# Optimization experiments

Hardware: AMD Instinct MI355X
Metric: run time of the kernel (lower is better)

## Reference

```python
import jax, jax.numpy as jnp
import numpy as np

N_NODES = 100000


def gcn_conv(x, src, dst, W, b, num_nodes):
    # PyG GCNConv: add self-loops, symmetric normalization D^-1/2 (A+I) D^-1/2, then linear.
    loop = jnp.arange(num_nodes, dtype=src.dtype)
    s = jnp.concatenate([src, loop])
    d = jnp.concatenate([dst, loop])
    deg = jax.ops.segment_sum(jnp.ones_like(d, dtype=x.dtype), d, num_segments=num_nodes)
    dinv = jnp.where(deg > 0, jax.lax.rsqrt(deg), 0.0)
    norm = dinv[s] * dinv[d]                       # [E+N]
    h = x @ W                                      # [N, out]
    msg = h[s] * norm[:, None]                     # gather + scale
    out = jax.ops.segment_sum(msg, d, num_segments=num_nodes)  # scatter-add
    return out + b


def setup_inputs() -> dict:
    key = jax.random.key(0)
    k1, k2, k3, k4 = jax.random.split(key, 4)
    F_IN, HID, C = 165, 128, 2
    E = 3200000
    x = jax.random.normal(k1, (N_NODES, F_IN), dtype=jnp.float32)
    edge_index = jax.random.randint(k2, (2, E), 0, N_NODES, dtype=jnp.int64)
    W1 = jax.random.normal(k3, (F_IN, HID), dtype=jnp.float32) * (1.0 / np.sqrt(F_IN))
    b1 = jnp.zeros((HID,), dtype=jnp.float32)
    W2 = jax.random.normal(k4, (HID, C), dtype=jnp.float32) * (1.0 / np.sqrt(HID))
    b2 = jnp.zeros((C,), dtype=jnp.float32)
    return {"x": x, "edge_index": edge_index, "W1": W1, "b1": b1, "W2": W2, "b2": b2}


def reference(x, edge_index, W1, b1, W2, b2):
    src, dst = edge_index[0], edge_index[1]
    h = jax.nn.relu(gcn_conv(x, src, dst, W1, b1, N_NODES))
    # dropout is identity in eval mode (self.training=False)
    out = gcn_conv(h, src, dst, W2, b2, N_NODES)
    return out
```

## Files before the change

kernel.cpp:

```cpp
#include <hip/hip_runtime.h>

#define NN  100000
#define FIN 165
#define HID 128
#define NBUCK 391
#define CHUNK 8192
#define CAP   9216
#define KPAD 192
#define WS   196

typedef __attribute__((ext_vector_type(4))) float f32x4;
typedef __attribute__((ext_vector_type(8))) short short8;

#define OFF_DINV   0
#define OFF_H1     100352
#define OFF_Z      (OFF_H1 + NN * 64)
#define OFF_ROWPTR (OFF_Z + 2 * NN)
#define OFF_GBASE  (OFF_ROWPTR + 100352)
#define OFF_GCUR   (OFF_GBASE + 512)
#define OFF_BUCK   (OFF_GCUR + 512)
#define OFF_EDATA  (OFF_BUCK + NBUCK * CAP)
#define OFF_WTHI   (OFF_EDATA + 3200000)

__device__ __forceinline__ unsigned bf16rne(float f) {
    unsigned u = __float_as_uint(f);
    return (u + 0x7FFFu + ((u >> 16) & 1u)) >> 16;
}

__device__ __forceinline__ float2 bf2_to_f2(unsigned int u) {
    float2 r;
    r.x = __uint_as_float(u << 16);
    r.y = __uint_as_float(u & 0xffff0000u);
    return r;
}

__device__ __forceinline__ short8 ldfrag(const ushort* p) {
    union { uint2 u[2]; short8 s; } f;
    f.u[0] = *(const uint2*)p;
    f.u[1] = *(const uint2*)(p + 16);
    return f.s;
}

__global__ void k_wsplit(const float* __restrict__ W1, ushort* __restrict__ hi,
                         int* __restrict__ gcur) {
    int t = blockIdx.x * blockDim.x + threadIdx.x;
    if (t < 512) gcur[t] = t * CAP;
    if (t >= HID * KPAD) return;
    int ch = t / KPAD, k = t % KPAD;
    float v = (k < FIN) ? W1[k * HID + ch] : 0.0f;
    hi[ch * KPAD + k] = (ushort)bf16rne(v);
}

__global__ __launch_bounds__(1024) void k_bfill(const int* __restrict__ src,
        const int* __restrict__ dst, int* __restrict__ gcur,
        unsigned int* __restrict__ bucketed, int ne) {
    __shared__ int hist[NBUCK];
    __shared__ int lcur[NBUCK];
    for (int i = threadIdx.x; i < NBUCK; i += 1024) hist[i] = 0;
    __syncthreads();
    const int4* dst4 = (const int4*)dst;
    const int4* src4 = (const int4*)src;
    const int ne4 = ne >> 2;
    const int base4 = blockIdx.x * (CHUNK / 4);
#pragma unroll
    for (int it = 0; it < CHUNK / 4096; ++it) {
        int e4 = base4 + it * 1024 + threadIdx.x;
        if (e4 < ne4) {
            int4 v = dst4[e4];
            atomicAdd(&hist[v.x >> 8], 1);
            atomicAdd(&hist[v.y >> 8], 1);
            atomicAdd(&hist[v.z >> 8], 1);
            atomicAdd(&hist[v.w >> 8], 1);
        }
    }
    if (blockIdx.x == 0 && threadIdx.x < (ne & 3))
        atomicAdd(&hist[dst[(ne & ~3) + threadIdx.x] >> 8], 1);
    __syncthreads();
    for (int i = threadIdx.x; i < NBUCK; i += 1024) {
        int h = hist[i];
        lcur[i] = h ? atomicAdd(&gcur[i], h) : 0;
    }
    __syncthreads();
#define PUT(D, S)                                                            \
    {                                                                        \
        int b_ = (D) >> 8;                                                   \
        int pos_ = atomicAdd(&lcur[b_], 1);                                  \
        if (pos_ < (b_ + 1) * CAP)                                           \
            bucketed[pos_] = (unsigned)(S) | ((unsigned)((D) & 255) << 24);  \
    }
#pragma unroll
    for (int it = 0; it < CHUNK / 4096; ++it) {
        int e4 = base4 + it * 1024 + threadIdx.x;
        if (e4 < ne4) {
            int4 d4 = dst4[e4];
            int4 s4 = src4[e4];
            PUT(d4.x, s4.x);
            PUT(d4.y, s4.y);
            PUT(d4.z, s4.z);
            PUT(d4.w, s4.w);
        }
    }
    if (blockIdx.x == 0 && threadIdx.x < (ne & 3)) {
        int e = (ne & ~3) + threadIdx.x;
        PUT(dst[e], src[e]);
    }
#undef PUT
}

__global__ __launch_bounds__(512) void k_bscan(const int* __restrict__ gcur,
        int* __restrict__ gbase) {
    __shared__ int s[512];
    int tid = threadIdx.x;
    int c = 0;
    if (tid < NBUCK) {
        c = gcur[tid] - tid * CAP;
        c = min(c, CAP);
    }
    s[tid] = c;
    __syncthreads();
    for (int off = 1; off < 512; off <<= 1) {
        int t = (tid >= off) ? s[tid - off] : 0;
        __syncthreads();
        s[tid] += t;
        __syncthreads();
    }
    if (tid < NBUCK) gbase[tid] = s[tid] - c;
    if (tid == NBUCK - 1) gbase[NBUCK] = s[tid];
}

__global__ __launch_bounds__(1024) void k_fine(const int* __restrict__ gbase,
        const unsigned int* __restrict__ bucketed, int* __restrict__ edata,
        int* __restrict__ rowptr, float* __restrict__ dinv, int n) {
    __shared__ int hist[256];
    __shared__ int scan[256];
    __shared__ int lcur[256];
    const int b = blockIdx.x;
    const int tid = threadIdx.x;
    const int rbeg = b * CAP;
    const int wbeg = gbase[b], wend = gbase[b + 1];
    const int cnt = wend - wbeg;
    if (tid < 256) hist[tid] = 0;
    __syncthreads();
    for (int j = tid; j < cnt; j += 1024)
        atomicAdd(&hist[bucketed[rbeg + j] >> 24], 1);
    __syncthreads();
    if (tid < 256) scan[tid] = hist[tid];
    __syncthreads();
    for (int off = 1; off < 256; off <<= 1) {
        int t = 0;
        if (tid < 256 && tid >= off) t = scan[tid - off];
        __syncthreads();
        if (tid < 256) scan[tid] += t;
        __syncthreads();
    }
    if (tid < 256) {
        int c = hist[tid];
        int excl = scan[tid] - c;
        int d = b * 256 + tid;
        if (d < n) {
            rowptr[d] = wbeg + excl;
            dinv[d] = rsqrtf((float)c + 1.0f);
        }
        lcur[tid] = wbeg + excl;
    }
    __syncthreads();
    for (int j = tid; j < cnt; j += 1024) {
        unsigned p = bucketed[rbeg + j];
        int pos = atomicAdd(&lcur[p >> 24], 1);
        edata[pos] = (int)(p & 0x00FFFFFFu);
    }
    if (b == NBUCK - 1 && tid == 0) rowptr[n] = wend;
}

__global__ __launch_bounds__(512) void k_gemm1(const float* __restrict__ x,
        const ushort* __restrict__ wthi, unsigned* __restrict__ h1, int n) {
    __shared__ alignas(16) ushort whi[128 * WS];
    const int tid = threadIdx.x;
    const int node0 = blockIdx.x * 128;
    const int wv = tid >> 6, lane = tid & 63;
    const int r15 = lane & 15, g = lane >> 4;

    {
        int ch = tid >> 2, q = tid & 3;
        int gb = ch * KPAD + q * 48;
        int lb = ch * WS + q * 48;
#pragma unroll
        for (int j = 0; j < 12; ++j) {
            uint2 v = *(const uint2*)&wthi[gb + j * 4];
            *(uint2*)&whi[lb + j * 4] = v;
        }
    }

    f32x4 acc[8];
#pragma unroll
    for (int ct = 0; ct < 8; ++ct) acc[ct] = (f32x4){0.f, 0.f, 0.f, 0.f};

    const int row = node0 + wv * 16 + r15;
    const bool rowok = row < n;
    const float* xrow = x + (size_t)row * FIN;

    __syncthreads();

    for (int ks = 0; ks < 6; ++ks) {
        unsigned hh[8];
#pragma unroll
        for (int j = 0; j < 4; ++j) {
            int k0 = ks * 32 + 4 * g + j;
            int k1 = k0 + 16;
            float v0 = (rowok && k0 < FIN) ? xrow[k0] : 0.0f;
            float v1 = (rowok && k1 < FIN) ? xrow[k1] : 0.0f;
            hh[j]     = bf16rne(v0);
            hh[4 + j] = bf16rne(v1);
        }
        union { unsigned u[4]; short8 s; } A;
        A.u[0] = hh[0] | (hh[1] << 16);
        A.u[1] = hh[2] | (hh[3] << 16);
        A.u[2] = hh[4] | (hh[5] << 16);
        A.u[3] = hh[6] | (hh[7] << 16);
#pragma unroll
        for (int ct = 0; ct < 8; ++ct) {
            short8 Bh = ldfrag(&whi[(ct * 16 + r15) * WS + ks * 32 + 4 * g]);
            acc[ct] = __builtin_amdgcn_mfma_f32_16x16x32_bf16(A.s, Bh, acc[ct], 0, 0, 0);
        }
    }

#pragma unroll
    for (int ct = 0; ct < 4; ++ct) {
#pragma unroll
        for (int r = 0; r < 4; ++r) {
            int node = node0 + wv * 16 + 4 * g + r;
            if (node < n) {
                unsigned p = bf16rne(acc[ct][r]) | (bf16rne(acc[ct + 4][r]) << 16);
                h1[node * 64 + ct * 16 + r15] = p;
            }
        }
    }
}

__global__ __launch_bounds__(256) void k_agg_fused(const int* __restrict__ rowptr,
        const int* __restrict__ edata, const unsigned int* __restrict__ h1,
        const float* __restrict__ dinv, const float* __restrict__ b1,
        const float* __restrict__ W2, float* __restrict__ z, int n0, int nn) {
    const int wid  = (blockIdx.x * blockDim.x + threadIdx.x) >> 6;
    const int lane = threadIdx.x & 63;
    if (wid >= nn) return;
    const int d = n0 + wid;
    const int beg = rowptr[d], end = rowptr[d + 1];
    const float di = dinv[d];
    const int grp = lane >> 4;
    const int sl  = lane & 15;

    float ax0, ax1, ax2, ax3, ay0, ay1, ay2, ay3;
    {
        uint4 hv = *(const uint4*)&h1[d * 64 + sl * 4];
        float nm = (grp == 0) ? di * di : 0.0f;
        float2 f0 = bf2_to_f2(hv.x), f1 = bf2_to_f2(hv.y);
        float2 f2 = bf2_to_f2(hv.z), f3 = bf2_to_f2(hv.w);
        ax0 = f0.x * nm; ay0 = f0.y * nm;
        ax1 = f1.x * nm; ay1 = f1.y * nm;
        ax2 = f2.x * nm; ay2 = f2.y * nm;
        ax3 = f3.x * nm; ay3 = f3.y * nm;
    }

#define PRELOAD(JB)                                                          \
    {                                                                        \
        int i0 = (JB) + grp, i1 = (JB) + 4 + grp,                            \
            i2 = (JB) + 8 + grp, i3 = (JB) + 12 + grp;                       \
        int c0 = min(i0, end - 1), c1 = min(i1, end - 1);                    \
        int c2 = min(i2, end - 1), c3 = min(i3, end - 1);                    \
        s0 = edata[c0]; s1 = edata[c1]; s2 = edata[c2]; s3 = edata[c3];      \
        m0 = (i0 < end) ? dinv[s0] * di : 0.0f;                              \
        m1 = (i1 < end) ? dinv[s1] * di : 0.0f;                              \
        m2 = (i2 < end) ? dinv[s2] * di : 0.0f;                              \
        m3 = (i3 < end) ? dinv[s3] * di : 0.0f;                              \
    }
#define ACC(G, NM)                                                           \
    {                                                                        \
        float2 f;                                                            \
        f = bf2_to_f2((G).x); ax0 = fmaf(f.x, (NM), ax0); ay0 = fmaf(f.y, (NM), ay0); \
        f = bf2_to_f2((G).y); ax1 = fmaf(f.x, (NM), ax1); ay1 = fmaf(f.y, (NM), ay1); \
        f = bf2_to_f2((G).z); ax2 = fmaf(f.x, (NM), ax2); ay2 = fmaf(f.y, (NM), ay2); \
        f = bf2_to_f2((G).w); ax3 = fmaf(f.x, (NM), ax3); ay3 = fmaf(f.y, (NM), ay3); \
    }

    if (beg < end) {
        int s0, s1, s2, s3;
        float m0, m1, m2, m3;
        PRELOAD(beg);
        for (int j = beg; j < end; j += 16) {
            uint4 g0 = *(const uint4*)&h1[s0 * 64 + sl * 4];
            uint4 g1 = *(const uint4*)&h1[s1 * 64 + sl * 4];
            uint4 g2 = *(const uint4*)&h1[s2 * 64 + sl * 4];
            uint4 g3 = *(const uint4*)&h1[s3 * 64 + sl * 4];
            float w0 = m0, w1 = m1, w2 = m2, w3 = m3;
            int jn = j + 16;
            if (jn < end) PRELOAD(jn);
            ACC(g0, w0); ACC(g1, w1); ACC(g2, w2); ACC(g3, w3);
        }
    }
#undef PRELOAD
#undef ACC

    ax0 += __shfl_xor(ax0, 16, 64); ax0 += __shfl_xor(ax0, 32, 64);
    ax1 += __shfl_xor(ax1, 16, 64); ax1 += __shfl_xor(ax1, 32, 64);
    ax2 += __shfl_xor(ax2, 16, 64); ax2 += __shfl_xor(ax2, 32, 64);
    ax3 += __shfl_xor(ax3, 16, 64); ax3 += __shfl_xor(ax3, 32, 64);
    ay0 += __shfl_xor(ay0, 16, 64); ay0 += __shfl_xor(ay0, 32, 64);
    ay1 += __shfl_xor(ay1, 16, 64); ay1 += __shfl_xor(ay1, 32, 64);
    ay2 += __shfl_xor(ay2, 16, 64); ay2 += __shfl_xor(ay2, 32, 64);
    ay3 += __shfl_xor(ay3, 16, 64); ay3 += __shfl_xor(ay3, 32, 64);
    const int c = sl * 4;
    float4 bA = *(const float4*)&b1[c];
    float4 bB = *(const float4*)&b1[c + 64];
    float v00 = ax0 + bA.x; v00 = v00 > 0.f ? v00 : 0.f;
    float v01 = ax1 + bA.y; v01 = v01 > 0.f ? v01 : 0.f;
    float v02 = ax2 + bA.z; v02 = v02 > 0.f ? v02 : 0.f;
    float v03 = ax3 + bA.w; v03 = v03 > 0.f ? v03 : 0.f;
    float v10 = ay0 + bB.x; v10 = v10 > 0.f ? v10 : 0.f;
    float v11 = ay1 + bB.y; v11 = v11 > 0.f ? v11 : 0.f;
    float v12 = ay2 + bB.z; v12 = v12 > 0.f ? v12 : 0.f;
    float v13 = ay3 + bB.w; v13 = v13 > 0.f ? v13 : 0.f;
    float4 wA0 = *(const float4*)&W2[c * 2];
    float4 wA1 = *(const float4*)&W2[c * 2 + 4];
    float4 wB0 = *(const float4*)&W2[(c + 64) * 2];
    float4 wB1 = *(const float4*)&W2[(c + 64) * 2 + 4];
    float p0 = v00 * wA0.x + v01 * wA0.z + v02 * wA1.x + v03 * wA1.z
             + v10 * wB0.x + v11 * wB0.z + v12 * wB1.x + v13 * wB1.z;
    float p1 = v00 * wA0.y + v01 * wA0.w + v02 * wA1.y + v03 * wA1.w
             + v10 * wB0.y + v11 * wB0.w + v12 * wB1.y + v13 * wB1.w;
#pragma unroll
    for (int m = 8; m >= 1; m >>= 1) {
        p0 += __shfl_xor(p0, m, 64);
        p1 += __shfl_xor(p1, m, 64);
    }
    if (lane == 0) *(float2*)&z[d * 2] = make_float2(p0, p1);
}

__global__ __launch_bounds__(256) void k_out(const int* __restrict__ rowptr,
        const int* __restrict__ edata, const float* __restrict__ z,
        const float* __restrict__ dinv, const float* __restrict__ b2,
        float* __restrict__ out, int n) {
    int g = (blockIdx.x * blockDim.x + threadIdx.x) >> 4;
    int l = threadIdx.x & 15;
    if (g >= n) return;
    int beg = rowptr[g], end = rowptr[g + 1];
    float di = dinv[g];
    float o0 = 0.0f, o1 = 0.0f;
    for (int j = beg + l; j < end; j += 16) {
        int s = edata[j];
        float nm = dinv[s] * di;
        float2 zs = *(const float2*)&z[s * 2];
        o0 = fmaf(zs.x, nm, o0);
        o1 = fmaf(zs.y, nm, o1);
    }
#pragma unroll
    for (int m = 8; m >= 1; m >>= 1) {
        o0 += __shfl_xor(o0, m, 16);
        o1 += __shfl_xor(o1, m, 16);
    }
    if (l == 0) {
        float2 zd = *(const float2*)&z[g * 2];
        float s2 = di * di;
        out[g * 2]     = fmaf(zd.x, s2, b2[0]) + o0;
        out[g * 2 + 1] = fmaf(zd.y, s2, b2[1]) + o1;
    }
}

extern "C" void kernel_launch(void* const* d_in, const int* in_sizes, int n_in,
                              void* d_out, int out_size, void* d_ws, size_t ws_size,
                              hipStream_t stream) {
    const float* x  = (const float*)d_in[0];
    const int*   ei = (const int*)d_in[1];
    const float* W1 = (const float*)d_in[2];
    const float* b1 = (const float*)d_in[3];
    const float* W2 = (const float*)d_in[4];
    const float* b2 = (const float*)d_in[5];
    float* out = (float*)d_out;

    const int n  = in_sizes[0] / FIN;
    const int ne = in_sizes[1] / 2;
    const int* src = ei;
    const int* dst = ei + ne;

    float* ws     = (float*)d_ws;
    float* dinv   = ws + OFF_DINV;
    unsigned int* h1 = (unsigned int*)(ws + OFF_H1);
    float* z      = ws + OFF_Z;
    int*   rowptr = (int*)(ws + OFF_ROWPTR);
    int*   gbase  = (int*)(ws + OFF_GBASE);
    int*   gcur   = (int*)(ws + OFF_GCUR);
    unsigned int* bucketed = (unsigned int*)(ws + OFF_BUCK);
    int*   edata  = (int*)(ws + OFF_EDATA);
    ushort* wthi  = (ushort*)(ws + OFF_WTHI);

    const int nchb = (ne + CHUNK - 1) / CHUNK;

    k_wsplit<<<(HID * KPAD + 255) / 256, 256, 0, stream>>>(W1, wthi, gcur);
    k_bfill<<<nchb, 1024, 0, stream>>>(src, dst, gcur, bucketed, ne);
    k_bscan<<<1, 512, 0, stream>>>(gcur, gbase);
    k_fine<<<NBUCK, 1024, 0, stream>>>(gbase, bucketed, edata, rowptr, dinv, n);
    k_gemm1<<<(n + 127) / 128, 512, 0, stream>>>(x, wthi, h1, n);
    const int q = (n + 3) / 4;
    for (int i = 0; i < 4; ++i) {
        int n0 = i * q;
        int nn = (n - n0 < q) ? (n - n0) : q;
        if (nn > 0)
            k_agg_fused<<<((size_t)nn * 64 + 255) / 256, 256, 0, stream>>>(
                rowptr, edata, h1, dinv, b1, W2, z, n0, nn);
    }
    k_out<<<(n * 16 + 255) / 256, 256, 0, stream>>>(rowptr, edata, z, dinv, b2, out, n);
}
```

Measured before the change: 256.1 us.

## Merge CSR fine-sort and GEMM1 into one launch; single aggregation launch

Combines the per-bucket fine sort (CSR build) and the first-layer GEMM into one kernel by giving the first NBUCK blocks the sort work and the remaining blocks the GEMM tiles. The two independent stages can then run concurrently on the GPU instead of back to back. The fine sort now uses 512 threads instead of 1024 and shares the GEMM's shared-memory allocation. The four chunked aggregation launches are also collapsed into one launch over all nodes, saving launch overhead but dropping whatever cache locality the chunking provided.

```diff
diff --git a/kernel.cpp b/kernel.cpp
--- a/kernel.cpp
+++ b/kernel.cpp
@@ -128,55 +128,60 @@
     if (tid == NBUCK - 1) gbase[NBUCK] = s[tid];
 }
 
-__global__ __launch_bounds__(1024) void k_fine(const int* __restrict__ gbase,
-        const unsigned int* __restrict__ bucketed, int* __restrict__ edata,
-        int* __restrict__ rowptr, float* __restrict__ dinv, int n) {
-    __shared__ int hist[256];
-    __shared__ int scan[256];
-    __shared__ int lcur[256];
-    const int b = blockIdx.x;
+__global__ __launch_bounds__(512) void k_fused2(
+        const float* __restrict__ x, const ushort* __restrict__ wthi,
+        unsigned* __restrict__ h1, int n,
+        const int* __restrict__ gbase, const unsigned int* __restrict__ bucketed,
+        int* __restrict__ edata, int* __restrict__ rowptr,
+        float* __restrict__ dinv) {
+    __shared__ alignas(16) unsigned char smem[128 * WS * 2];
+
+    if (blockIdx.x < NBUCK) {
+        int* hist = (int*)smem;
+        int* scan = hist + 256;
+        int* lcur = scan + 256;
+        const int b = blockIdx.x;
+        const int tid = threadIdx.x;
+        const int rbeg = b * CAP;
+        const int wbeg = gbase[b], wend = gbase[b + 1];
+        const int cnt = wend - wbeg;
+        if (tid < 256) hist[tid] = 0;
+        __syncthreads();
+        for (int j = tid; j < cnt; j += 512)
+            atomicAdd(&hist[bucketed[rbeg + j] >> 24], 1);
+        __syncthreads();
+        if (tid < 256) scan[tid] = hist[tid];
+        __syncthreads();
+        for (int off = 1; off < 256; off <<= 1) {
+            int t = 0;
+            if (tid < 256 && tid >= off) t = scan[tid - off];
+            __syncthreads();
+            if (tid < 256) scan[tid] += t;
+            __syncthreads();
+        }
+        if (tid < 256) {
+            int c = hist[tid];
+            int excl = scan[tid] - c;
+            int d = b * 256 + tid;
+            if (d < n) {
+                rowptr[d] = wbeg + excl;
+                dinv[d] = rsqrtf((float)c + 1.0f);
+            }
+            lcur[tid] = wbeg + excl;
+        }
+        __syncthreads();
+        for (int j = tid; j < cnt; j += 512) {
+            unsigned p = bucketed[rbeg + j];
+            int pos = atomicAdd(&lcur[p >> 24], 1);
+            edata[pos] = (int)(p & 0x00FFFFFFu);
+        }
+        if (b == NBUCK - 1 && tid == 0) rowptr[n] = wend;
+        return;
+    }
+
+    ushort* whi = (ushort*)smem;
     const int tid = threadIdx.x;
-    const int rbeg = b * CAP;
-    const int wbeg = gbase[b], wend = gbase[b + 1];
-    const int cnt = wend - wbeg;
-    if (tid < 256) hist[tid] = 0;
-    __syncthreads();
-    for (int j = tid; j < cnt; j += 1024)
-        atomicAdd(&hist[bucketed[rbeg + j] >> 24], 1);
-    __syncthreads();
-    if (tid < 256) scan[tid] = hist[tid];
-    __syncthreads();
-    for (int off = 1; off < 256; off <<= 1) {
-        int t = 0;
-        if (tid < 256 && tid >= off) t = scan[tid - off];
-        __syncthreads();
-        if (tid < 256) scan[tid] += t;
-        __syncthreads();
-    }
-    if (tid < 256) {
-        int c = hist[tid];
-        int excl = scan[tid] - c;
-        int d = b * 256 + tid;
-        if (d < n) {
-            rowptr[d] = wbeg + excl;
-            dinv[d] = rsqrtf((float)c + 1.0f);
-        }
-        lcur[tid] = wbeg + excl;
-    }
-    __syncthreads();
-    for (int j = tid; j < cnt; j += 1024) {
-        unsigned p = bucketed[rbeg + j];
-        int pos = atomicAdd(&lcur[p >> 24], 1);
-        edata[pos] = (int)(p & 0x00FFFFFFu);
-    }
-    if (b == NBUCK - 1 && tid == 0) rowptr[n] = wend;
-}
-
-__global__ __launch_bounds__(512) void k_gemm1(const float* __restrict__ x,
-        const ushort* __restrict__ wthi, unsigned* __restrict__ h1, int n) {
-    __shared__ alignas(16) ushort whi[128 * WS];
-    const int tid = threadIdx.x;
-    const int node0 = blockIdx.x * 128;
+    const int node0 = (blockIdx.x - NBUCK) * 128;
     const int wv = tid >> 6, lane = tid & 63;
     const int r15 = lane & 15, g = lane >> 4;
 
@@ -191,13 +196,13 @@
         }
     }
 
-    f32x4 acc[8];
-#pragma unroll
-    for (int ct = 0; ct < 8; ++ct) acc[ct] = (f32x4){0.f, 0.f, 0.f, 0.f};
-
     const int row = node0 + wv * 16 + r15;
     const bool rowok = row < n;
     const float* xrow = x + (size_t)row * FIN;
+
+    f32x4 acc[8];
+#pragma unroll
+    for (int ct = 0; ct < 8; ++ct) acc[ct] = (f32x4){0.f, 0.f, 0.f, 0.f};
 
     __syncthreads();
 
@@ -240,11 +245,11 @@
 __global__ __launch_bounds__(256) void k_agg_fused(const int* __restrict__ rowptr,
         const int* __restrict__ edata, const unsigned int* __restrict__ h1,
         const float* __restrict__ dinv, const float* __restrict__ b1,
-        const float* __restrict__ W2, float* __restrict__ z, int n0, int nn) {
+        const float* __restrict__ W2, float* __restrict__ z, int n) {
     const int wid  = (blockIdx.x * blockDim.x + threadIdx.x) >> 6;
     const int lane = threadIdx.x & 63;
-    if (wid >= nn) return;
-    const int d = n0 + wid;
+    if (wid >= n) return;
+    const int d = wid;
     const int beg = rowptr[d], end = rowptr[d + 1];
     const float di = dinv[d];
     const int grp = lane >> 4;
@@ -393,20 +398,15 @@
     int*   edata  = (int*)(ws + OFF_EDATA);
     ushort* wthi  = (ushort*)(ws + OFF_WTHI);
 
-    const int nchb = (ne + CHUNK - 1) / CHUNK;
+    const int nchb  = (ne + CHUNK - 1) / CHUNK;
+    const int ngemm = (n + 127) / 128;
 
     k_wsplit<<<(HID * KPAD + 255) / 256, 256, 0, stream>>>(W1, wthi, gcur);
     k_bfill<<<nchb, 1024, 0, stream>>>(src, dst, gcur, bucketed, ne);
     k_bscan<<<1, 512, 0, stream>>>(gcur, gbase);
-    k_fine<<<NBUCK, 1024, 0, stream>>>(gbase, bucketed, edata, rowptr, dinv, n);
-    k_gemm1<<<(n + 127) / 128, 512, 0, stream>>>(x, wthi, h1, n);
-    const int q = (n + 3) / 4;
-    for (int i = 0; i < 4; ++i) {
-        int n0 = i * q;
-        int nn = (n - n0 < q) ? (n - n0) : q;
-        if (nn > 0)
-            k_agg_fused<<<((size_t)nn * 64 + 255) / 256, 256, 0, stream>>>(
-                rowptr, edata, h1, dinv, b1, W2, z, n0, nn);
-    }
+    k_fused2<<<NBUCK + ngemm, 512, 0, stream>>>(x, wthi, h1, n,
+                                                gbase, bucketed, edata, rowptr, dinv);
+    k_agg_fused<<<((size_t)n * 64 + 255) / 256, 256, 0, stream>>>(
+        rowptr, edata, h1, dinv, b1, W2, z, n);
     k_out<<<(n * 16 + 255) / 256, 256, 0, stream>>>(rowptr, edata, z, dinv, b2, out, n);
 }
```

Result: faster. 227.5 us (-11.2%).
